# Kernel tuning notes

Measured on AMD Instinct MI355X. Metric: run time of the kernel, lower is better.

## Reference

```python
import jax, jax.numpy as jnp
import numpy as np

NUM_EMBEDDINGS = 1024
EMBEDDING_DIM = 64
COMMITMENT_COST = 0.25


def setup_inputs() -> dict:
    key = jax.random.key(0)
    k_x, k_cb = jax.random.split(key)
    x = jax.random.normal(k_x, (16, EMBEDDING_DIM, 64, 64), dtype=jnp.float32)
    # nn.Embedding weight init: uniform(-1/K, 1/K)
    codebook = jax.random.uniform(
        k_cb, (NUM_EMBEDDINGS, EMBEDDING_DIM), dtype=jnp.float32,
        minval=-1.0 / NUM_EMBEDDINGS, maxval=1.0 / NUM_EMBEDDINGS)
    return {"x": x, "codebook": codebook}


def reference(x, codebook):
    sg = jax.lax.stop_gradient
    # NCHW -> NHWC
    inputs = jnp.transpose(x, (0, 2, 3, 1))  # [B,H,W,D]
    in_shape = inputs.shape
    flat = inputs.reshape(-1, EMBEDDING_DIM)  # [N,D]
    # squared L2 distances to each codebook entry: [N,K]
    distances = (jnp.sum(flat ** 2, axis=1, keepdims=True)
                 + jnp.sum(codebook ** 2, axis=1)
                 - 2.0 * jnp.matmul(flat, codebook.T))
    encoding_indices = jnp.argmin(distances, axis=1)  # [N]
    # one-hot matmul in the original == plain gather
    quantized = codebook[encoding_indices].reshape(in_shape)  # [B,H,W,D]
    e_latent_loss = jnp.mean((sg(quantized) - inputs) ** 2)
    q_latent_loss = jnp.mean((quantized - sg(inputs)) ** 2)
    loss = q_latent_loss + COMMITMENT_COST * e_latent_loss
    # straight-through estimator
    quantized = inputs + sg(quantized - inputs)
    quantized = jnp.transpose(quantized, (0, 3, 1, 2))  # NHWC -> NCHW
    return quantized, loss
```

## Files before the change

### kernel.cpp

```cpp
#include <hip/hip_runtime.h>

#define NPTS   65536
#define DIM    64
#define KCODES 1024
#define HW     4096
#define CH     128
#define NCH    8
#define ROWP   72

typedef __attribute__((ext_vector_type(8))) short  short8;
typedef __attribute__((ext_vector_type(4))) float  floatx4;

__device__ __forceinline__ short f2bf(float f) {
    unsigned u = __builtin_bit_cast(unsigned, f);
    u = (u + 0x7FFFu + ((u >> 16) & 1u)) >> 16;
    return (short)u;
}

__global__ __launch_bounds__(512, 4) void vq_fused(
    const float* __restrict__ x, const float* __restrict__ cb,
    float* __restrict__ out, float* __restrict__ loss_ptr)
{
    __shared__ __align__(16) short s_cb[CH * ROWP];
    __shared__ float s_cbn[CH];
    __shared__ float s_part[2][128];
    __shared__ float s_xn[128];
    __shared__ float s_red[2];

    const int tid  = threadIdx.x;
    const int lane = tid & 63;
    const int wave = tid >> 6;
    const int col  = lane & 15;
    const int quad = lane >> 4;
    const int pg   = wave & 3;
    const int kc   = wave >> 2;

    const int pb = blockIdx.x * 128 + pg * 32;
    short8 afrag[2][2];
    #pragma unroll
    for (int pt = 0; pt < 2; ++pt) {
        int n = pb + pt * 16 + col;
        const float* bp = x + ((size_t)(n >> 12) << 18) + (n & 4095);
        float ns = 0.0f;
        #pragma unroll
        for (int kh = 0; kh < 2; ++kh) {
            short8 f;
            #pragma unroll
            for (int j = 0; j < 8; ++j) {
                float v = bp[(size_t)(kh * 32 + quad * 8 + j) * HW];
                f[j] = f2bf(v);
                ns = fmaf(v, v, ns);
            }
            afrag[pt][kh] = f;
        }
        ns += __shfl_xor(ns, 16, 64);
        ns += __shfl_xor(ns, 32, 64);
        if (kc == 0 && quad == 0) s_xn[pg * 32 + pt * 16 + col] = ns;
    }

    float best[2][4];
    #pragma unroll
    for (int pt = 0; pt < 2; ++pt)
        #pragma unroll
        for (int r = 0; r < 4; ++r) best[pt][r] = -3.4e38f;

    for (int c = 0; c < NCH; ++c) {
        __syncthreads();
        #pragma unroll
        for (int i = 0; i < 2; ++i) {
            int g = tid + 512 * i;
            const float4* p4 = (const float4*)cb + (size_t)c * 2048 + 2 * g;
            float4 va = p4[0], vb = p4[1];
            short8 v;
            v[0] = f2bf(va.x); v[1] = f2bf(va.y); v[2] = f2bf(va.z); v[3] = f2bf(va.w);
            v[4] = f2bf(vb.x); v[5] = f2bf(vb.y); v[6] = f2bf(vb.z); v[7] = f2bf(vb.w);
            int cc = g >> 3, part = g & 7;
            *(short8*)&s_cb[cc * ROWP + part * 8] = v;
            float ns = fmaf(va.x, va.x, fmaf(va.y, va.y, fmaf(va.z, va.z, va.w * va.w)));
            ns = fmaf(vb.x, vb.x, fmaf(vb.y, vb.y, fmaf(vb.z, vb.z, fmaf(vb.w, vb.w, ns))));
            ns += __shfl_xor(ns, 1, 64);
            ns += __shfl_xor(ns, 2, 64);
            ns += __shfl_xor(ns, 4, 64);
            if ((tid & 7) == 0) s_cbn[cc] = -0.5f * ns;
        }
        __syncthreads();
        #pragma unroll
        for (int ct = 0; ct < 4; ++ct) {
            int cc = kc * 64 + ct * 16 + col;
            float initv = s_cbn[cc];
            unsigned idxv = (unsigned)(c * CH + cc);
            const short* rp = &s_cb[cc * ROWP + quad * 8];
            short8 b0 = *(const short8*)rp;
            short8 b1 = *(const short8*)(rp + 32);
            floatx4 cinit = {initv, initv, initv, initv};
            #pragma unroll
            for (int pt = 0; pt < 2; ++pt) {
                floatx4 acc = __builtin_amdgcn_mfma_f32_16x16x32_bf16(afrag[pt][0], b0, cinit, 0, 0, 0);
                acc = __builtin_amdgcn_mfma_f32_16x16x32_bf16(afrag[pt][1], b1, acc, 0, 0, 0);
                #pragma unroll
                for (int r = 0; r < 4; ++r) {
                    unsigned pbits = (__builtin_bit_cast(unsigned, acc[r]) & 0xFFFFFC00u) | idxv;
                    best[pt][r] = fmaxf(best[pt][r], __builtin_bit_cast(float, pbits));
                }
            }
        }
    }

    #pragma unroll
    for (int pt = 0; pt < 2; ++pt)
        #pragma unroll
        for (int r = 0; r < 4; ++r) {
            float v = best[pt][r];
            v = fmaxf(v, __shfl_xor(v, 1, 64));
            v = fmaxf(v, __shfl_xor(v, 2, 64));
            v = fmaxf(v, __shfl_xor(v, 4, 64));
            v = fmaxf(v, __shfl_xor(v, 8, 64));
            best[pt][r] = v;
        }
    if (col == 0) {
        #pragma unroll
        for (int pt = 0; pt < 2; ++pt)
            #pragma unroll
            for (int r = 0; r < 4; ++r)
                s_part[kc][pg * 32 + pt * 16 + quad * 4 + r] = best[pt][r];
    }
    __syncthreads();

    {
        int ptid = tid & 127;
        int dq   = tid >> 7;
        float m = fmaxf(s_part[0][ptid], s_part[1][ptid]);
        unsigned mu = __builtin_bit_cast(unsigned, m);
        int idx = (int)(mu & 1023u);
        int n = blockIdx.x * 128 + ptid;
        float* op = out + ((size_t)(n >> 12) << 18) + (n & 4095);
        const float4* crow = (const float4*)(cb + (size_t)idx * DIM + dq * 16);
        #pragma unroll
        for (int j = 0; j < 4; ++j) {
            float4 v = crow[j];
            op[(size_t)(dq * 16 + j * 4 + 0) * HW] = v.x;
            op[(size_t)(dq * 16 + j * 4 + 1) * HW] = v.y;
            op[(size_t)(dq * 16 + j * 4 + 2) * HW] = v.z;
            op[(size_t)(dq * 16 + j * 4 + 3) * HW] = v.w;
        }
        if (dq == 0) {
            float vtr = __builtin_bit_cast(float, mu & 0xFFFFFC00u);
            float lp = s_xn[ptid] - 2.0f * vtr;
            #pragma unroll
            for (int off = 32; off > 0; off >>= 1)
                lp += __shfl_down(lp, off, 64);
            if (lane == 0) s_red[wave] = lp;
        }
    }
    __syncthreads();
    if (tid == 0)
        atomicAdd(loss_ptr, (s_red[0] + s_red[1]) * (1.25f / ((float)NPTS * DIM)));
}

extern "C" void kernel_launch(void* const* d_in, const int* in_sizes, int n_in,
                              void* d_out, int out_size, void* d_ws, size_t ws_size,
                              hipStream_t stream) {
    const float* x  = (const float*)d_in[0];
    const float* cb = (const float*)d_in[1];
    float* out      = (float*)d_out;
    float* loss_ptr = out + (size_t)NPTS * DIM;

    vq_fused<<<NPTS / 128, 512, 0, stream>>>(x, cb, out, loss_ptr);
}
```

Baseline: 91.22 us.

## Precompute bf16 codebook and norms in prep kernel, read directly from global

Adds a small prep kernel that converts the codebook to bf16 and computes the scaled code norms into workspace once per call. The main kernel then loads codebook fragments straight from global memory (L2-resident) instead of having every block convert and stage 128-code chunks in LDS with two barriers per chunk. This removes the redundant per-block conversion work and the block-wide syncs. In exchange it adds a second launch and relies on global/L2 latency being hidden inside the MFMA loop.

New measurement: 106.5 us. 16.8% more time.

```diff
diff --git a/kernel.cpp b/kernel.cpp
--- a/kernel.cpp
+++ b/kernel.cpp
@@ -4,9 +4,6 @@
 #define DIM    64
 #define KCODES 1024
 #define HW     4096
-#define CH     128
-#define NCH    8
-#define ROWP   72
 
 typedef __attribute__((ext_vector_type(8))) short  short8;
 typedef __attribute__((ext_vector_type(4))) float  floatx4;
@@ -17,12 +14,30 @@
     return (short)u;
 }
 
-__global__ __launch_bounds__(512, 4) void vq_fused(
+__global__ __launch_bounds__(256) void vq_prep(
+    const float* __restrict__ cb, short* __restrict__ cbb,
+    float* __restrict__ nrm)
+{
+    int g = blockIdx.x * 256 + threadIdx.x;
+    const float4* p = (const float4*)cb + 2 * (size_t)g;
+    float4 a = p[0], b = p[1];
+    short8 v;
+    v[0] = f2bf(a.x); v[1] = f2bf(a.y); v[2] = f2bf(a.z); v[3] = f2bf(a.w);
+    v[4] = f2bf(b.x); v[5] = f2bf(b.y); v[6] = f2bf(b.z); v[7] = f2bf(b.w);
+    *(short8*)(cbb + 8 * (size_t)g) = v;
+    float ns = fmaf(a.x, a.x, fmaf(a.y, a.y, fmaf(a.z, a.z, a.w * a.w)));
+    ns = fmaf(b.x, b.x, fmaf(b.y, b.y, fmaf(b.z, b.z, fmaf(b.w, b.w, ns))));
+    ns += __shfl_xor(ns, 1, 64);
+    ns += __shfl_xor(ns, 2, 64);
+    ns += __shfl_xor(ns, 4, 64);
+    if ((g & 7) == 0) nrm[g >> 3] = -0.5f * ns;
+}
+
+__global__ __launch_bounds__(512, 4) void vq_main(
     const float* __restrict__ x, const float* __restrict__ cb,
+    const short* __restrict__ cbb, const float* __restrict__ nrm,
     float* __restrict__ out, float* __restrict__ loss_ptr)
 {
-    __shared__ __align__(16) short s_cb[CH * ROWP];
-    __shared__ float s_cbn[CH];
     __shared__ float s_part[2][128];
     __shared__ float s_xn[128];
     __shared__ float s_red[2];
@@ -64,44 +79,24 @@
         #pragma unroll
         for (int r = 0; r < 4; ++r) best[pt][r] = -3.4e38f;
 
-    for (int c = 0; c < NCH; ++c) {
-        __syncthreads();
+    const int cb0 = kc * 512;
+    #pragma unroll 4
+    for (int ct = 0; ct < 32; ++ct) {
+        int code = cb0 + ct * 16 + col;
+        const short* rp = cbb + (code << 6) + (quad << 3);
+        short8 b0 = *(const short8*)rp;
+        short8 b1 = *(const short8*)(rp + 32);
+        float nv = nrm[code];
+        floatx4 cinit = {nv, nv, nv, nv};
+        unsigned idxv = (unsigned)code;
         #pragma unroll
-        for (int i = 0; i < 2; ++i) {
-            int g = tid + 512 * i;
-            const float4* p4 = (const float4*)cb + (size_t)c * 2048 + 2 * g;
-            float4 va = p4[0], vb = p4[1];
-            short8 v;
-            v[0] = f2bf(va.x); v[1] = f2bf(va.y); v[2] = f2bf(va.z); v[3] = f2bf(va.w);
-            v[4] = f2bf(vb.x); v[5] = f2bf(vb.y); v[6] = f2bf(vb.z); v[7] = f2bf(vb.w);
-            int cc = g >> 3, part = g & 7;
-            *(short8*)&s_cb[cc * ROWP + part * 8] = v;
-            float ns = fmaf(va.x, va.x, fmaf(va.y, va.y, fmaf(va.z, va.z, va.w * va.w)));
-            ns = fmaf(vb.x, vb.x, fmaf(vb.y, vb.y, fmaf(vb.z, vb.z, fmaf(vb.w, vb.w, ns))));
-            ns += __shfl_xor(ns, 1, 64);
-            ns += __shfl_xor(ns, 2, 64);
-            ns += __shfl_xor(ns, 4, 64);
-            if ((tid & 7) == 0) s_cbn[cc] = -0.5f * ns;
-        }
-        __syncthreads();
-        #pragma unroll
-        for (int ct = 0; ct < 4; ++ct) {
-            int cc = kc * 64 + ct * 16 + col;
-            float initv = s_cbn[cc];
-            unsigned idxv = (unsigned)(c * CH + cc);
-            const short* rp = &s_cb[cc * ROWP + quad * 8];
-            short8 b0 = *(const short8*)rp;
-            short8 b1 = *(const short8*)(rp + 32);
-            floatx4 cinit = {initv, initv, initv, initv};
+        for (int pt = 0; pt < 2; ++pt) {
+            floatx4 acc = __builtin_amdgcn_mfma_f32_16x16x32_bf16(afrag[pt][0], b0, cinit, 0, 0, 0);
+            acc = __builtin_amdgcn_mfma_f32_16x16x32_bf16(afrag[pt][1], b1, acc, 0, 0, 0);
             #pragma unroll
-            for (int pt = 0; pt < 2; ++pt) {
-                floatx4 acc = __builtin_amdgcn_mfma_f32_16x16x32_bf16(afrag[pt][0], b0, cinit, 0, 0, 0);
-                acc = __builtin_amdgcn_mfma_f32_16x16x32_bf16(afrag[pt][1], b1, acc, 0, 0, 0);
-                #pragma unroll
-                for (int r = 0; r < 4; ++r) {
-                    unsigned pbits = (__builtin_bit_cast(unsigned, acc[r]) & 0xFFFFFC00u) | idxv;
-                    best[pt][r] = fmaxf(best[pt][r], __builtin_bit_cast(float, pbits));
-                }
+            for (int r = 0; r < 4; ++r) {
+                unsigned pbits = (__builtin_bit_cast(unsigned, acc[r]) & 0xFFFFFC00u) | idxv;
+                best[pt][r] = fmaxf(best[pt][r], __builtin_bit_cast(float, pbits));
             }
         }
     }
@@ -165,5 +160,9 @@
     float* out      = (float*)d_out;
     float* loss_ptr = out + (size_t)NPTS * DIM;
 
-    vq_fused<<<NPTS / 128, 512, 0, stream>>>(x, cb, out, loss_ptr);
+    short* cbb = (short*)d_ws;
+    float* nrm = (float*)((char*)d_ws + (size_t)KCODES * DIM * sizeof(short));
+
+    vq_prep<<<32, 256, 0, stream>>>(cb, cbb, nrm);
+    vq_main<<<NPTS / 128, 512, 0, stream>>>(x, cb, cbb, nrm, out, loss_ptr);
 }
```

## Stage full bf16 codebook in LDS once and double points per block

Applied to the files above, without the earlier changes.

The kernel now converts and stores the entire 1024-entry codebook in shared memory (128 KB, XOR-swizzled rows instead of padding) in a single pass, removing the eight per-chunk barrier-separated staging phases. Each block handles 256 points instead of 128, with each wave holding four A fragments, which halves the number of times the codebook is re-read and converted across the grid. The cost is much larger LDS use per block, which limits occupancy (launch bounds lowered to 2), and a larger register footprint for the accumulators. Only 256 blocks are launched, so the whole fill happens up front with no overlap against compute.

Result: faster. 89.37 us (-2.0%).

```diff
diff --git a/kernel.cpp b/kernel.cpp
--- a/kernel.cpp
+++ b/kernel.cpp
@@ -4,9 +4,6 @@
 #define DIM    64
 #define KCODES 1024
 #define HW     4096
-#define CH     128
-#define NCH    8
-#define ROWP   72
 
 typedef __attribute__((ext_vector_type(8))) short  short8;
 typedef __attribute__((ext_vector_type(4))) float  floatx4;
@@ -17,15 +14,15 @@
     return (short)u;
 }
 
-__global__ __launch_bounds__(512, 4) void vq_fused(
+__global__ __launch_bounds__(512, 2) void vq_fused(
     const float* __restrict__ x, const float* __restrict__ cb,
     float* __restrict__ out, float* __restrict__ loss_ptr)
 {
-    __shared__ __align__(16) short s_cb[CH * ROWP];
-    __shared__ float s_cbn[CH];
-    __shared__ float s_part[2][128];
-    __shared__ float s_xn[128];
-    __shared__ float s_red[2];
+    __shared__ __align__(16) short s_cb[KCODES * DIM];
+    __shared__ float s_nrm[KCODES];
+    __shared__ float s_part[2][256];
+    __shared__ float s_xn[256];
+    __shared__ float s_red[4];
 
     const int tid  = threadIdx.x;
     const int lane = tid & 63;
@@ -35,10 +32,28 @@
     const int pg   = wave & 3;
     const int kc   = wave >> 2;
 
-    const int pb = blockIdx.x * 128 + pg * 32;
-    short8 afrag[2][2];
     #pragma unroll
-    for (int pt = 0; pt < 2; ++pt) {
+    for (int i = 0; i < 16; ++i) {
+        int g = tid + 512 * i;
+        int c = g >> 3, p = g & 7;
+        const float4* p4 = (const float4*)cb + 2 * (size_t)g;
+        float4 va = p4[0], vb = p4[1];
+        short8 v;
+        v[0] = f2bf(va.x); v[1] = f2bf(va.y); v[2] = f2bf(va.z); v[3] = f2bf(va.w);
+        v[4] = f2bf(vb.x); v[5] = f2bf(vb.y); v[6] = f2bf(vb.z); v[7] = f2bf(vb.w);
+        *(short8*)&s_cb[(c << 6) + ((p ^ (c & 7)) << 3)] = v;
+        float ns = fmaf(va.x, va.x, fmaf(va.y, va.y, fmaf(va.z, va.z, va.w * va.w)));
+        ns = fmaf(vb.x, vb.x, fmaf(vb.y, vb.y, fmaf(vb.z, vb.z, fmaf(vb.w, vb.w, ns))));
+        ns += __shfl_xor(ns, 1, 64);
+        ns += __shfl_xor(ns, 2, 64);
+        ns += __shfl_xor(ns, 4, 64);
+        if ((g & 7) == 0) s_nrm[c] = -0.5f * ns;
+    }
+
+    const int pb = blockIdx.x * 256 + pg * 64;
+    short8 afrag[4][2];
+    #pragma unroll
+    for (int pt = 0; pt < 4; ++pt) {
         int n = pb + pt * 16 + col;
         const float* bp = x + ((size_t)(n >> 12) << 18) + (n & 4095);
         float ns = 0.0f;
@@ -55,59 +70,42 @@
         }
         ns += __shfl_xor(ns, 16, 64);
         ns += __shfl_xor(ns, 32, 64);
-        if (kc == 0 && quad == 0) s_xn[pg * 32 + pt * 16 + col] = ns;
+        if (kc == 0 && quad == 0) s_xn[pg * 64 + pt * 16 + col] = ns;
     }
 
-    float best[2][4];
+    __syncthreads();
+
+    float best[4][4];
     #pragma unroll
-    for (int pt = 0; pt < 2; ++pt)
+    for (int pt = 0; pt < 4; ++pt)
         #pragma unroll
         for (int r = 0; r < 4; ++r) best[pt][r] = -3.4e38f;
 
-    for (int c = 0; c < NCH; ++c) {
-        __syncthreads();
+    const int cb0 = kc * 512;
+    #pragma unroll 4
+    for (int ct = 0; ct < 32; ++ct) {
+        int code = cb0 + ct * 16 + col;
+        int c7 = code & 7;
+        int so = code << 6;
+        short8 b0 = *(const short8*)&s_cb[so + (((quad    ) ^ c7) << 3)];
+        short8 b1 = *(const short8*)&s_cb[so + (((quad + 4) ^ c7) << 3)];
+        float nv = s_nrm[code];
+        floatx4 cinit = {nv, nv, nv, nv};
+        unsigned idxv = (unsigned)code;
         #pragma unroll
-        for (int i = 0; i < 2; ++i) {
-            int g = tid + 512 * i;
-            const float4* p4 = (const float4*)cb + (size_t)c * 2048 + 2 * g;
-            float4 va = p4[0], vb = p4[1];
-            short8 v;
-            v[0] = f2bf(va.x); v[1] = f2bf(va.y); v[2] = f2bf(va.z); v[3] = f2bf(va.w);
-            v[4] = f2bf(vb.x); v[5] = f2bf(vb.y); v[6] = f2bf(vb.z); v[7] = f2bf(vb.w);
-            int cc = g >> 3, part = g & 7;
-            *(short8*)&s_cb[cc * ROWP + part * 8] = v;
-            float ns = fmaf(va.x, va.x, fmaf(va.y, va.y, fmaf(va.z, va.z, va.w * va.w)));
-            ns = fmaf(vb.x, vb.x, fmaf(vb.y, vb.y, fmaf(vb.z, vb.z, fmaf(vb.w, vb.w, ns))));
-            ns += __shfl_xor(ns, 1, 64);
-            ns += __shfl_xor(ns, 2, 64);
-            ns += __shfl_xor(ns, 4, 64);
-            if ((tid & 7) == 0) s_cbn[cc] = -0.5f * ns;
-        }
-        __syncthreads();
-        #pragma unroll
-        for (int ct = 0; ct < 4; ++ct) {
-            int cc = kc * 64 + ct * 16 + col;
-            float initv = s_cbn[cc];
-            unsigned idxv = (unsigned)(c * CH + cc);
-            const short* rp = &s_cb[cc * ROWP + quad * 8];
-            short8 b0 = *(const short8*)rp;
-            short8 b1 = *(const short8*)(rp + 32);
-            floatx4 cinit = {initv, initv, initv, initv};
+        for (int pt = 0; pt < 4; ++pt) {
+            floatx4 acc = __builtin_amdgcn_mfma_f32_16x16x32_bf16(afrag[pt][0], b0, cinit, 0, 0, 0);
+            acc = __builtin_amdgcn_mfma_f32_16x16x32_bf16(afrag[pt][1], b1, acc, 0, 0, 0);
             #pragma unroll
-            for (int pt = 0; pt < 2; ++pt) {
-                floatx4 acc = __builtin_amdgcn_mfma_f32_16x16x32_bf16(afrag[pt][0], b0, cinit, 0, 0, 0);
-                acc = __builtin_amdgcn_mfma_f32_16x16x32_bf16(afrag[pt][1], b1, acc, 0, 0, 0);
-                #pragma unroll
-                for (int r = 0; r < 4; ++r) {
-                    unsigned pbits = (__builtin_bit_cast(unsigned, acc[r]) & 0xFFFFFC00u) | idxv;
-                    best[pt][r] = fmaxf(best[pt][r], __builtin_bit_cast(float, pbits));
-                }
+            for (int r = 0; r < 4; ++r) {
+                unsigned pbits = (__builtin_bit_cast(unsigned, acc[r]) & 0xFFFFFC00u) | idxv;
+                best[pt][r] = fmaxf(best[pt][r], __builtin_bit_cast(float, pbits));
             }
         }
     }
 
     #pragma unroll
-    for (int pt = 0; pt < 2; ++pt)
+    for (int pt = 0; pt < 4; ++pt)
         #pragma unroll
         for (int r = 0; r < 4; ++r) {
             float v = best[pt][r];
@@ -119,29 +117,29 @@
         }
     if (col == 0) {
         #pragma unroll
-        for (int pt = 0; pt < 2; ++pt)
+        for (int pt = 0; pt < 4; ++pt)
             #pragma unroll
             for (int r = 0; r < 4; ++r)
-                s_part[kc][pg * 32 + pt * 16 + quad * 4 + r] = best[pt][r];
+                s_part[kc][pg * 64 + pt * 16 + quad * 4 + r] = best[pt][r];
     }
     __syncthreads();
 
     {
-        int ptid = tid & 127;
-        int dq   = tid >> 7;
+        int ptid = tid & 255;
+        int dq   = tid >> 8;
         float m = fmaxf(s_part[0][ptid], s_part[1][ptid]);
         unsigned mu = __builtin_bit_cast(unsigned, m);
         int idx = (int)(mu & 1023u);
-        int n = blockIdx.x * 128 + ptid;
+        int n = blockIdx.x * 256 + ptid;
         float* op = out + ((size_t)(n >> 12) << 18) + (n & 4095);
-        const float4* crow = (const float4*)(cb + (size_t)idx * DIM + dq * 16);
+        const float4* crow = (const float4*)(cb + (size_t)idx * DIM + dq * 32);
         #pragma unroll
-        for (int j = 0; j < 4; ++j) {
+        for (int j = 0; j < 8; ++j) {
             float4 v = crow[j];
-            op[(size_t)(dq * 16 + j * 4 + 0) * HW] = v.x;
-            op[(size_t)(dq * 16 + j * 4 + 1) * HW] = v.y;
-            op[(size_t)(dq * 16 + j * 4 + 2) * HW] = v.z;
-            op[(size_t)(dq * 16 + j * 4 + 3) * HW] = v.w;
+            op[(size_t)(dq * 32 + j * 4 + 0) * HW] = v.x;
+            op[(size_t)(dq * 32 + j * 4 + 1) * HW] = v.y;
+            op[(size_t)(dq * 32 + j * 4 + 2) * HW] = v.z;
+            op[(size_t)(dq * 32 + j * 4 + 3) * HW] = v.w;
         }
         if (dq == 0) {
             float vtr = __builtin_bit_cast(float, mu & 0xFFFFFC00u);
@@ -154,7 +152,8 @@
     }
     __syncthreads();
     if (tid == 0)
-        atomicAdd(loss_ptr, (s_red[0] + s_red[1]) * (1.25f / ((float)NPTS * DIM)));
+        atomicAdd(loss_ptr, (s_red[0] + s_red[1] + s_red[2] + s_red[3])
+                              * (1.25f / ((float)NPTS * DIM)));
 }
 
 extern "C" void kernel_launch(void* const* d_in, const int* in_sizes, int n_in,
@@ -165,5 +164,5 @@
     float* out      = (float*)d_out;
     float* loss_ptr = out + (size_t)NPTS * DIM;
 
-    vq_fused<<<NPTS / 128, 512, 0, stream>>>(x, cb, out, loss_ptr);
+    vq_fused<<<NPTS / 256, 512, 0, stream>>>(x, cb, out, loss_ptr);
 }
```
